# Kernel optimization log

Hardware: AMD Instinct MI355X
Metric: run time of the kernel (lower is better)

## Reference

```python
import jax, jax.numpy as jnp
import numpy as np

B, S, D = 1, 2048, 2048
H = 32          # num_heads == num_kv_heads (n_rep = 1)
QB = 8          # rosa_num_query_key_bits
VB = 8          # rosa_num_value_bits
TAU = 1.0


def setup_inputs() -> dict:
    key = jax.random.key(0)
    ks = jax.random.split(key, 8)
    s = 0.02
    return {
        "hidden_states": jax.random.normal(ks[0], (B, S, D), dtype=jnp.float32),
        "Wq": jax.random.normal(ks[1], (D, H * QB), dtype=jnp.float32) * s,
        "Wk": jax.random.normal(ks[2], (D, H * QB), dtype=jnp.float32) * s,
        "Wv": jax.random.normal(ks[3], (D, H * VB), dtype=jnp.float32) * s,
        "Wo": jax.random.normal(ks[4], (H * VB, D), dtype=jnp.float32) * s,
        "Wg": jax.random.normal(ks[5], (D, D), dtype=jnp.float32) * s,
        "v_emb0": jnp.full((H * VB,), -1e-05, dtype=jnp.float32),
        "v_emb1": jnp.full((H * VB,), +1e-05, dtype=jnp.float32),
    }


def _rosa_attention(hs, Wq, Wk, Wv, Wo, Wg, v_emb0, v_emb1):
    b, s, _ = hs.shape
    # low-bit projections -> [B, H, S, bits]
    q = (hs @ Wq).reshape(b, s, H, QB).transpose(0, 2, 1, 3)
    k = (hs @ Wk).reshape(b, s, H, QB).transpose(0, 2, 1, 3)
    v = (hs @ Wv).reshape(b, s, H, VB).transpose(0, 2, 1, 3)
    # soft-binarized bit probabilities (training-mode relaxation, temperature tau)
    pq = jax.nn.sigmoid(q / TAU)
    pk = jax.nn.sigmoid(k / TAU)
    pv = jax.nn.sigmoid(v / TAU)
    # expected number of matching bits:
    # sum_d pq*pk + (1-pq)*(1-pk) = 2*<pq,pk> - sum(pq) - sum(pk) + QB
    dot = jnp.einsum('bhqd,bhkd->bhqk', pq, pk)
    scores = 2.0 * dot - pq.sum(-1)[..., :, None] - pk.sum(-1)[..., None, :] + QB
    # causal mask
    causal = jnp.tril(jnp.ones((s, s), dtype=bool))
    scores = jnp.where(causal, scores / TAU, jnp.finfo(scores.dtype).min)
    attn = jax.nn.softmax(scores, axis=-1)
    out = jnp.einsum('bhqk,bhkd->bhqd', attn, pv)           # [B,H,S,VB], in (0,1)
    out = out.transpose(0, 2, 1, 3).reshape(b, s, H * VB)
    # binary value-embedding interpolation
    out = v_emb1 * out + v_emb0 * (1.0 - out)
    out = out @ Wo
    gate = jax.nn.sigmoid(hs @ Wg)
    return out * gate


def reference(hidden_states, Wq, Wk, Wv, Wo, Wg, v_emb0, v_emb1):
    return _rosa_attention(hidden_states, Wq, Wk, Wv, Wo, Wg, v_emb0, v_emb1)
```

## Files before the change

### kernel.cpp

```cpp
#include <hip/hip_runtime.h>

#define S 2048
#define DIM 2048
#define H 32
#define NB 2816
#define SA 25.0f
#define SW 1150.0f

using u16 = unsigned short;
using u8 = unsigned char;
using short8 = __attribute__((ext_vector_type(8))) short;
using f32x4 = __attribute__((ext_vector_type(4))) float;
using i32x4 = __attribute__((ext_vector_type(4))) int;

__device__ __forceinline__ u16 f2bf(float x) {
  union { float f; unsigned u; } v; v.f = x;
  unsigned r = v.u + 0x7fffu + ((v.u >> 16) & 1u);
  return (u16)(r >> 16);
}
__device__ __forceinline__ float bf2f(u16 x) {
  union { unsigned u; float f; } v; v.u = ((unsigned)x) << 16; return v.f;
}
__device__ __forceinline__ int clampi(int x) { return x < -127 ? -127 : (x > 127 ? 127 : x); }
__device__ __forceinline__ unsigned q4i8(float a, float b, float c, float d, float s) {
  int x0 = clampi((int)rintf(a * s)), x1 = clampi((int)rintf(b * s));
  int x2 = clampi((int)rintf(c * s)), x3 = clampi((int)rintf(d * s));
  return (x0 & 255) | ((x1 & 255) << 8) | ((x2 & 255) << 16) | ((unsigned)(x3 & 255) << 24);
}

#define GLOAD_LDS16(g, l)                                                      \
  __builtin_amdgcn_global_load_lds(                                            \
      (const __attribute__((address_space(1))) unsigned*)(g),                  \
      (__attribute__((address_space(3))) unsigned*)(l), 16, 0, 0)

__global__ __launch_bounds__(256)
void trans_all_k(const float* __restrict__ Wq, const float* __restrict__ Wk,
                 const float* __restrict__ Wv, const float* __restrict__ Wg,
                 const float* __restrict__ Wo, const float* __restrict__ hs,
                 u16* __restrict__ Wt, u8* __restrict__ Wg8, u16* __restrict__ Wot,
                 u16* __restrict__ Abf, u8* __restrict__ A8) {
  int b = blockIdx.x;
  const int t = threadIdx.x;
  if (b >= 1536) {
    int i = ((b - 1536) * 256 + t) * 8;
    float4 a = *(const float4*)(hs + i);
    float4 c = *(const float4*)(hs + i + 4);
    uint4 r;
    r.x = f2bf(a.x) | ((unsigned)f2bf(a.y) << 16);
    r.y = f2bf(a.z) | ((unsigned)f2bf(a.w) << 16);
    r.z = f2bf(c.x) | ((unsigned)f2bf(c.y) << 16);
    r.w = f2bf(c.z) | ((unsigned)f2bf(c.w) << 16);
    int row = i >> 11, k = i & 2047;
    int dst = (row << 11) + (k & ~63) + ((((k >> 3) & 7) ^ (row & 7)) << 3);
    *(uint4*)(Abf + dst) = r;
    uint2 q;
    q.x = q4i8(a.x, a.y, a.z, a.w, SA);
    q.y = q4i8(c.x, c.y, c.z, c.w, SA);
    int dst8 = (row << 11) + (k & ~63) + ((((k >> 4) & 3) ^ (row & 3)) << 4) + (k & 8);
    *(uint2*)(A8 + dst8) = q;
    return;
  }
  const float* in; int K, N;
  int mode;
  u16* out = nullptr;
  if (b < 384) {
    K = 2048; N = 256; mode = 0;
    in = (b < 128) ? Wq : (b < 256) ? Wk : Wv;
    out = Wt + (size_t)(b >> 7) * 256 * 2048;
    b &= 127;
  } else if (b < 1408) {
    in = Wg; mode = 1; K = 2048; N = 2048; b -= 384;
  } else {
    in = Wo; out = Wot; mode = 2; K = 256; N = 2048; b -= 1408;
  }
  const int nbN = N >> 6;
  const int kb = (b / nbN) << 6, nb = (b % nbN) << 6;
  __shared__ float tile[64][65];
  const int n4 = (t & 15) * 4;
#pragma unroll
  for (int p = 0; p < 4; p++) {
    int k = p * 16 + (t >> 4);
    float4 v = *(const float4*)(in + (size_t)(kb + k) * N + nb + n4);
    tile[k][n4] = v.x; tile[k][n4 + 1] = v.y; tile[k][n4 + 2] = v.z; tile[k][n4 + 3] = v.w;
  }
  __syncthreads();
  const int k8 = (t & 7) * 8;
#pragma unroll
  for (int p = 0; p < 2; p++) {
    int n = p * 32 + (t >> 3);
    if (mode == 1) {
      int nr = nb + n;
      uint2 w;
      w.x = q4i8(tile[k8 + 0][n], tile[k8 + 1][n], tile[k8 + 2][n], tile[k8 + 3][n], SW);
      w.y = q4i8(tile[k8 + 4][n], tile[k8 + 5][n], tile[k8 + 6][n], tile[k8 + 7][n], SW);
      int col = kb + ((((k8 >> 4) ^ (nr & 3))) << 4) + (k8 & 8);
      *(uint2*)(Wg8 + (size_t)nr * 2048 + col) = w;
    } else {
      uint4 w;
      w.x = f2bf(tile[k8 + 0][n]) | ((unsigned)f2bf(tile[k8 + 1][n]) << 16);
      w.y = f2bf(tile[k8 + 2][n]) | ((unsigned)f2bf(tile[k8 + 3][n]) << 16);
      w.z = f2bf(tile[k8 + 4][n]) | ((unsigned)f2bf(tile[k8 + 5][n]) << 16);
      w.w = f2bf(tile[k8 + 6][n]) | ((unsigned)f2bf(tile[k8 + 7][n]) << 16);
      if (mode == 2) {
        *(uint4*)(out + (size_t)(nb + n) * K + kb + k8) = w;
      } else {
        int nr = nb + n;
        int col = kb + ((((k8 >> 3) ^ (nr & 7))) << 3);
        *(uint4*)(out + (size_t)nr * 2048 + col) = w;
      }
    }
  }
}

__global__ __launch_bounds__(256)
void gemm1_mix_k(const u16* __restrict__ Abf, const u16* __restrict__ Wt,
                 const u8* __restrict__ A8, const u8* __restrict__ Wg8,
                 u16* __restrict__ Pb) {
  __shared__ __align__(16) char smem[65536];
  const int t = threadIdx.x;
  const int f = blockIdx.x;
  int bn, bm;
  if (f >= 160 && f < 256) {
    int g = f - 160;
    bn = g % 6;  bm = (g / 6) * 128;
  } else {
    int g = (f < 160) ? f : f - 96;
    bn = 6 + (g & 15);  bm = (g >> 4) * 128;
  }
  const int wave = t >> 6, lane = t & 63;
  const int wm = (wave >> 1) * 64, wn = (wave & 1) * 64;
  const int l16 = lane & 15, quad = lane >> 4;
  const int K = 2048;
  const int srow = t >> 3;
  if (bn < 6) {
    typedef u16 (*Tile)[128][64];
    Tile As = (Tile)smem;
    Tile Bs = (Tile)(smem + 32768);
    const int scol = (t & 7) * 8;
    const u16* Ap = Abf + (size_t)(bm + srow) * K + scol;
    const u16* Bp = Wt + (size_t)(bn * 128 + srow) * K + scol;
#define STAGE1(buf, koff)                                                      \
  do {                                                                         \
    GLOAD_LDS16(Ap + (koff), &As[buf][srow][scol]);                            \
    GLOAD_LDS16(Ap + 32 * (size_t)K + (koff), &As[buf][srow + 32][scol]);      \
    GLOAD_LDS16(Ap + 64 * (size_t)K + (koff), &As[buf][srow + 64][scol]);      \
    GLOAD_LDS16(Ap + 96 * (size_t)K + (koff), &As[buf][srow + 96][scol]);      \
    GLOAD_LDS16(Bp + (koff), &Bs[buf][srow][scol]);                            \
    GLOAD_LDS16(Bp + 32 * (size_t)K + (koff), &Bs[buf][srow + 32][scol]);      \
    GLOAD_LDS16(Bp + 64 * (size_t)K + (koff), &Bs[buf][srow + 64][scol]);      \
    GLOAD_LDS16(Bp + 96 * (size_t)K + (koff), &Bs[buf][srow + 96][scol]);      \
  } while (0)
    f32x4 acc[4][4];
#pragma unroll
    for (int i = 0; i < 4; i++)
#pragma unroll
      for (int j = 0; j < 4; j++) acc[i][j] = (f32x4){0.f, 0.f, 0.f, 0.f};
    STAGE1(0, 0);
    for (int kk = 0; kk < K; kk += 64) {
      const int cur = (kk >> 6) & 1, nxt = cur ^ 1;
      __syncthreads();
      if (kk + 64 < K) STAGE1(nxt, kk + 64);
      short8 af[4][2], bf[4][2];
#pragma unroll
      for (int mt = 0; mt < 4; mt++) {
        int row = wm + mt * 16 + l16;
        int rs = (row & 7) << 3;
        af[mt][0] = *(const short8*)&As[cur][row][(quad << 3) ^ rs];
        af[mt][1] = *(const short8*)&As[cur][row][((quad + 4) << 3) ^ rs];
      }
#pragma unroll
      for (int nt = 0; nt < 4; nt++) {
        int row = wn + nt * 16 + l16;
        int rs = (row & 7) << 3;
        bf[nt][0] = *(const short8*)&Bs[cur][row][(quad << 3) ^ rs];
        bf[nt][1] = *(const short8*)&Bs[cur][row][((quad + 4) << 3) ^ rs];
      }
#pragma unroll
      for (int mt = 0; mt < 4; mt++)
#pragma unroll
        for (int nt = 0; nt < 4; nt++) {
          acc[mt][nt] = __builtin_amdgcn_mfma_f32_16x16x32_bf16(af[mt][0], bf[nt][0], acc[mt][nt], 0, 0, 0);
          acc[mt][nt] = __builtin_amdgcn_mfma_f32_16x16x32_bf16(af[mt][1], bf[nt][1], acc[mt][nt], 0, 0, 0);
        }
    }
#pragma unroll
    for (int mt = 0; mt < 4; mt++)
#pragma unroll
      for (int nt = 0; nt < 4; nt++)
#pragma unroll
        for (int r = 0; r < 4; r++) {
          int m = bm + wm + mt * 16 + quad * 4 + r;
          int n = bn * 128 + wn + nt * 16 + l16;
          float v = acc[mt][nt][r];
          Pb[(size_t)m * NB + n] = f2bf(1.f / (1.f + __expf(-v)));
        }
#undef STAGE1
  } else {
    typedef u8 (*TileG)[128][128];
    TileG As = (TileG)smem;
    TileG Bs = (TileG)(smem + 32768);
    const int scol = (t & 7) * 16;
    const u8* Ap = A8 + (size_t)(bm + srow) * K + scol;
    const u8* Bp = Wg8 + (size_t)((bn - 6) * 128 + srow) * K + scol;
#define STAGEG(buf, koff)                                                      \
  do {                                                                         \
    GLOAD_LDS16(Ap + (koff), &As[buf][srow][scol]);                            \
    GLOAD_LDS16(Ap + 32 * (size_t)K + (koff), &As[buf][srow + 32][scol]);      \
    GLOAD_LDS16(Ap + 64 * (size_t)K + (koff), &As[buf][srow + 64][scol]);      \
    GLOAD_LDS16(Ap + 96 * (size_t)K + (koff), &As[buf][srow + 96][scol]);      \
    GLOAD_LDS16(Bp + (koff), &Bs[buf][srow][scol]);                            \
    GLOAD_LDS16(Bp + 32 * (size_t)K + (koff), &Bs[buf][srow + 32][scol]);      \
    GLOAD_LDS16(Bp + 64 * (size_t)K + (koff), &Bs[buf][srow + 64][scol]);      \
    GLOAD_LDS16(Bp + 96 * (size_t)K + (koff), &Bs[buf][srow + 96][scol]);      \
  } while (0)
    i32x4 acc[4][4];
#pragma unroll
    for (int i = 0; i < 4; i++)
#pragma unroll
      for (int j = 0; j < 4; j++) acc[i][j] = (i32x4){0, 0, 0, 0};
    STAGEG(0, 0);
    for (int kk = 0; kk < K; kk += 128) {
      const int cur = (kk >> 7) & 1, nxt = cur ^ 1;
      __syncthreads();
      if (kk + 128 < K) STAGEG(nxt, kk + 128);
      i32x4 af[4][2], bf[4][2];
#pragma unroll
      for (int mt = 0; mt < 4; mt++) {
        int row = wm + mt * 16 + l16;
        int sl = (quad ^ (row & 3)) << 4;
        af[mt][0] = *(const i32x4*)&As[cur][row][sl];
        af[mt][1] = *(const i32x4*)&As[cur][row][64 + sl];
      }
#pragma unroll
      for (int nt = 0; nt < 4; nt++) {
        int row = wn + nt * 16 + l16;
        int sl = (quad ^ (row & 3)) << 4;
        bf[nt][0] = *(const i32x4*)&Bs[cur][row][sl];
        bf[nt][1] = *(const i32x4*)&Bs[cur][row][64 + sl];
      }
#pragma unroll
      for (int mt = 0; mt < 4; mt++)
#pragma unroll
        for (int nt = 0; nt < 4; nt++) {
          acc[mt][nt] = __builtin_amdgcn_mfma_i32_16x16x64_i8(af[mt][0], bf[nt][0], acc[mt][nt], 0, 0, 0);
          acc[mt][nt] = __builtin_amdgcn_mfma_i32_16x16x64_i8(af[mt][1], bf[nt][1], acc[mt][nt], 0, 0, 0);
        }
    }
    const float inv = 1.f / (SA * SW);
#pragma unroll
    for (int mt = 0; mt < 4; mt++)
#pragma unroll
      for (int nt = 0; nt < 4; nt++)
#pragma unroll
        for (int r = 0; r < 4; r++) {
          int m = bm + wm + mt * 16 + quad * 4 + r;
          int n = bn * 128 + wn + nt * 16 + l16;
          float v = (float)acc[mt][nt][r] * inv;
          Pb[(size_t)m * NB + n] = f2bf(1.f / (1.f + __expf(-v)));
        }
#undef STAGEG
  }
}

__global__ __launch_bounds__(256)
void gemm64_k(const u16* __restrict__ A, const u16* __restrict__ Bt,
              float* __restrict__ C, const u16* __restrict__ gate,
              int K, int ldc) {
  __shared__ u16 As[2][64][32];
  __shared__ u16 Bs[2][64][32];
  const int t = threadIdx.x;
  const int bm = blockIdx.y * 64, bn = blockIdx.x * 64;
  const int wave = t >> 6, lane = t & 63;
  const int wm = (wave >> 1) * 32, wn = (wave & 1) * 32;
  const int l16 = lane & 15, quad = lane >> 4;
  const int srow = t >> 2, scol = (t & 3) * 8;
  const u16* Ap = A + (size_t)(bm + srow) * K + scol;
  const u16* Bp = Bt + (size_t)(bn + srow) * K + scol;
  f32x4 acc[2][2];
#pragma unroll
  for (int i = 0; i < 2; i++)
#pragma unroll
    for (int j = 0; j < 2; j++) acc[i][j] = (f32x4){0.f, 0.f, 0.f, 0.f};
  GLOAD_LDS16(Ap, &As[0][srow][scol]);
  GLOAD_LDS16(Bp, &Bs[0][srow][scol]);
  for (int kk = 0; kk < K; kk += 32) {
    const int cur = (kk >> 5) & 1, nxt = cur ^ 1;
    __syncthreads();
    if (kk + 32 < K) {
      GLOAD_LDS16(Ap + kk + 32, &As[nxt][srow][scol]);
      GLOAD_LDS16(Bp + kk + 32, &Bs[nxt][srow][scol]);
    }
    short8 af[2], bf[2];
#pragma unroll
    for (int mt = 0; mt < 2; mt++) af[mt] = *(const short8*)&As[cur][wm + mt * 16 + l16][quad * 8];
#pragma unroll
    for (int nt = 0; nt < 2; nt++) bf[nt] = *(const short8*)&Bs[cur][wn + nt * 16 + l16][quad * 8];
#pragma unroll
    for (int mt = 0; mt < 2; mt++)
#pragma unroll
      for (int nt = 0; nt < 2; nt++)
        acc[mt][nt] = __builtin_amdgcn_mfma_f32_16x16x32_bf16(af[mt], bf[nt], acc[mt][nt], 0, 0, 0);
  }
#pragma unroll
  for (int mt = 0; mt < 2; mt++)
#pragma unroll
    for (int nt = 0; nt < 2; nt++)
#pragma unroll
      for (int r = 0; r < 4; r++) {
        int m = bm + wm + mt * 16 + quad * 4 + r;
        int n = bn + wn + nt * 16 + l16;
        float v = acc[mt][nt][r] * bf2f(gate[(size_t)m * NB + n]);
        C[(size_t)m * ldc + n] = v;
      }
}

__global__ __launch_bounds__(256)
void attn_mfma_k(const u16* __restrict__ P, float* __restrict__ Part) {
  __shared__ u16 Plds[128 * 128];
  __shared__ u16 Vt[16 * 264];
  __shared__ u16 Klds[256 * 8];
  __shared__ u16 Qlds[128 * 8];
  __shared__ float sk2[256];
  const int h = blockIdx.y;
  int tau = blockIdx.x, m = 0;
  while (tau >= (m >> 1) + 1) { tau -= (m >> 1) + 1; m++; }
  const int kc = tau;
  const bool needMask = (kc == (m >> 1));
  const int q0 = m * 128, kb = kc * 256;
  const int t = threadIdx.x, wave = t >> 6, lane = t & 63;
  const int l16 = lane & 15, quad = lane >> 4;
  if (t < 128) {
    *(uint4*)&Qlds[t * 8] = *(const uint4*)(P + (size_t)(q0 + t) * NB + h * 8);
  }
  {
    const u16* rk = P + (size_t)(kb + t) * NB + 256 + h * 8;
    uint4 wk = *(const uint4*)rk;
    uint4 wv = *(const uint4*)(rk + 256);
    const u16* kv = (const u16*)&wk;
    float sum = 0.f;
#pragma unroll
    for (int d = 0; d < 8; d++) sum += bf2f(kv[d]);
    sk2[t] = sum * 1.44269504f;
    *(uint4*)&Klds[t * 8] = wk;
    const u16* vv = (const u16*)&wv;
#pragma unroll
    for (int d = 0; d < 8; d++) Vt[d * 264 + t] = vv[d];
    Vt[8 * 264 + t] = 0x3F80;
#pragma unroll
    for (int d = 9; d < 16; d++) Vt[d * 264 + t] = 0;
  }
  __syncthreads();
  short8 bq[2];
#pragma unroll
  for (int i = 0; i < 2; i++) {
    short8 z = {0, 0, 0, 0, 0, 0, 0, 0};
    if (quad == 0) z = *(const short8*)&Qlds[((wave * 2 + i) * 16 + l16) * 8];
    bq[i] = z;
  }
  f32x4 O[2];
  O[0] = (f32x4){0.f, 0.f, 0.f, 0.f};
  O[1] = (f32x4){0.f, 0.f, 0.f, 0.f};
  const int nsl = needMask ? (m & 1) + 1 : 2;
  const int swz = (l16 >> 1) & 7;
  for (int sl = 0; sl < nsl; sl++) {
    const int ks = sl * 128;
    const bool dm = needMask && (sl == (m & 1));
    for (int kt = 0; kt < 8; kt++) {
      short8 ak = {0, 0, 0, 0, 0, 0, 0, 0};
      if (quad == 0) ak = *(const short8*)&Klds[(ks + kt * 16 + l16) * 8];
      float4 s2 = *(const float4*)&sk2[ks + kt * 16 + quad * 4];
#pragma unroll
      for (int i = 0; i < 2; i++) {
        f32x4 c = __builtin_amdgcn_mfma_f32_16x16x32_bf16(
            ak, bq[i], (f32x4){0.f, 0.f, 0.f, 0.f}, 0, 0, 0);
        float e0 = exp2f(c[0] * 2.88539008f - s2.x);
        float e1 = exp2f(c[1] * 2.88539008f - s2.y);
        float e2 = exp2f(c[2] * 2.88539008f - s2.z);
        float e3 = exp2f(c[3] * 2.88539008f - s2.w);
        if (dm) {
          int q = q0 + (wave * 2 + i) * 16 + l16;
          int key = kb + ks + kt * 16 + quad * 4;
          e0 = (key + 0 <= q) ? e0 : 0.f;
          e1 = (key + 1 <= q) ? e1 : 0.f;
          e2 = (key + 2 <= q) ? e2 : 0.f;
          e3 = (key + 3 <= q) ? e3 : 0.f;
        }
        uint2 pk2;
        pk2.x = f2bf(e0) | ((unsigned)f2bf(e1) << 16);
        pk2.y = f2bf(e2) | ((unsigned)f2bf(e3) << 16);
        int row = (wave * 2 + i) * 16 + l16;
        int cb = 2 * kt + (quad >> 1);
        int pb = cb ^ swz;
        *(uint2*)&Plds[row * 128 + pb * 8 + (quad & 1) * 4] = pk2;
      }
    }
#pragma unroll
    for (int kc4 = 0; kc4 < 4; kc4++) {
      short8 bv = *(const short8*)&Vt[l16 * 264 + ks + kc4 * 32 + quad * 8];
#pragma unroll
      for (int i = 0; i < 2; i++) {
        int row = (wave * 2 + i) * 16 + l16;
        int pb = (kc4 * 4 + quad) ^ swz;
        short8 ap = *(const short8*)&Plds[row * 128 + pb * 8];
        O[i] = __builtin_amdgcn_mfma_f32_16x16x32_bf16(ap, bv, O[i], 0, 0, 0);
      }
    }
  }
  if (l16 < 9) {
#pragma unroll
    for (int i = 0; i < 2; i++) {
      int qb = q0 + (wave * 2 + i) * 16 + quad * 4;
#pragma unroll
      for (int r = 0; r < 4; r++)
        Part[(((size_t)h * S + qb + r) * 8 + kc) * 12 + l16] = O[i][r];
    }
  }
}

__global__ __launch_bounds__(256)
void attn_merge_k(const float* __restrict__ Part, const float* __restrict__ e0,
                  const float* __restrict__ e1, u16* __restrict__ O2) {
  const int q = blockIdx.x;
  const int t = threadIdx.x;
  const int d = t & 7;
  const int nch = (q >> 8) + 1;
  size_t base = ((size_t)(t >> 3) * S + q) * 8 * 12;
  float ov = 0.f, lv = 0.f;
  for (int kc = 0; kc < nch; kc++) {
    ov += Part[base + (size_t)kc * 12 + d];
    lv += Part[base + (size_t)kc * 12 + 8];
  }
  float outv = ov / lv;
  float r = e0[t] + (e1[t] - e0[t]) * outv;
  O2[(size_t)q * 256 + t] = f2bf(r);
}

extern "C" void kernel_launch(void* const* d_in, const int* in_sizes, int n_in,
                              void* d_out, int out_size, void* d_ws, size_t ws_size,
                              hipStream_t stream) {
  const float* hs = (const float*)d_in[0];
  const float* Wq = (const float*)d_in[1];
  const float* Wk = (const float*)d_in[2];
  const float* Wv = (const float*)d_in[3];
  const float* Wo = (const float*)d_in[4];
  const float* Wg = (const float*)d_in[5];
  const float* e0 = (const float*)d_in[6];
  const float* e1 = (const float*)d_in[7];
  float* out = (float*)d_out;
  char* ws = (char*)d_ws;
  u16*   Abf  = (u16*)(ws + 0);
  u8*    A8   = (u8*)(ws + 8388608);
  u16*   Wt   = (u16*)(ws + 12582912);
  u8*    Wg8  = (u8*)(ws + 15728640);
  u16*   Wot  = (u16*)(ws + 19922944);
  u16*   O2   = (u16*)(ws + 20971520);
  u16*   Pb   = (u16*)(ws + 22020096);
  float* Part = (float*)(ws + 33554432);

  trans_all_k<<<dim3(3584), 256, 0, stream>>>(Wq, Wk, Wv, Wg, Wo, hs, Wt, Wg8, Wot, Abf, A8);
  gemm1_mix_k<<<dim3(352), 256, 0, stream>>>(Abf, Wt, A8, Wg8, Pb);
  attn_mfma_k<<<dim3(72, H), 256, 0, stream>>>(Pb, Part);
  attn_merge_k<<<dim3(S), 256, 0, stream>>>(Part, e0, e1, O2);
  gemm64_k<<<dim3(DIM / 64, S / 64), 256, 0, stream>>>(O2, Wot, out, Pb + 768, 256, DIM);
}
```

Measured before the change: 168.5 us.

## Fuse attention split-K partials and merge into single kernel with in-block K loop

Replaces the split-K attention kernel plus separate merge kernel with one kernel where each block loops over all key chunks for its 128-query tile and head, accumulating in registers. The final normalization and value-embedding interpolation are done in-kernel using a lane shuffle to fetch the row-sum column. Blocks are ordered so the heaviest query tiles launch first. This removes the partial-sum buffer writes/reads and one kernel launch, but cuts the grid from 2304 to 512 blocks with uneven per-block work, which lowers parallelism and may leave the GPU underfilled.

```diff
diff --git a/kernel.cpp b/kernel.cpp
--- a/kernel.cpp
+++ b/kernel.cpp
@@ -315,40 +315,22 @@
 }
 
 __global__ __launch_bounds__(256)
-void attn_mfma_k(const u16* __restrict__ P, float* __restrict__ Part) {
+void attn_fused_k(const u16* __restrict__ P, const float* __restrict__ e0,
+                  const float* __restrict__ e1, u16* __restrict__ O2) {
   __shared__ u16 Plds[128 * 128];
   __shared__ u16 Vt[16 * 264];
   __shared__ u16 Klds[256 * 8];
   __shared__ u16 Qlds[128 * 8];
   __shared__ float sk2[256];
-  const int h = blockIdx.y;
-  int tau = blockIdx.x, m = 0;
-  while (tau >= (m >> 1) + 1) { tau -= (m >> 1) + 1; m++; }
-  const int kc = tau;
-  const bool needMask = (kc == (m >> 1));
-  const int q0 = m * 128, kb = kc * 256;
+  const int f = blockIdx.x;
+  int h, m;
+  if (f < 256) { h = f >> 3; m = 8 + (f & 7); }
+  else         { int g = f - 256; h = g >> 3; m = 7 - (g & 7); }
+  const int q0 = m * 128;
   const int t = threadIdx.x, wave = t >> 6, lane = t & 63;
   const int l16 = lane & 15, quad = lane >> 4;
-  if (t < 128) {
+  if (t < 128)
     *(uint4*)&Qlds[t * 8] = *(const uint4*)(P + (size_t)(q0 + t) * NB + h * 8);
-  }
-  {
-    const u16* rk = P + (size_t)(kb + t) * NB + 256 + h * 8;
-    uint4 wk = *(const uint4*)rk;
-    uint4 wv = *(const uint4*)(rk + 256);
-    const u16* kv = (const u16*)&wk;
-    float sum = 0.f;
-#pragma unroll
-    for (int d = 0; d < 8; d++) sum += bf2f(kv[d]);
-    sk2[t] = sum * 1.44269504f;
-    *(uint4*)&Klds[t * 8] = wk;
-    const u16* vv = (const u16*)&wv;
-#pragma unroll
-    for (int d = 0; d < 8; d++) Vt[d * 264 + t] = vv[d];
-    Vt[8 * 264 + t] = 0x3F80;
-#pragma unroll
-    for (int d = 9; d < 16; d++) Vt[d * 264 + t] = 0;
-  }
   __syncthreads();
   short8 bq[2];
 #pragma unroll
@@ -360,79 +342,90 @@
   f32x4 O[2];
   O[0] = (f32x4){0.f, 0.f, 0.f, 0.f};
   O[1] = (f32x4){0.f, 0.f, 0.f, 0.f};
-  const int nsl = needMask ? (m & 1) + 1 : 2;
   const int swz = (l16 >> 1) & 7;
-  for (int sl = 0; sl < nsl; sl++) {
-    const int ks = sl * 128;
-    const bool dm = needMask && (sl == (m & 1));
-    for (int kt = 0; kt < 8; kt++) {
-      short8 ak = {0, 0, 0, 0, 0, 0, 0, 0};
-      if (quad == 0) ak = *(const short8*)&Klds[(ks + kt * 16 + l16) * 8];
-      float4 s2 = *(const float4*)&sk2[ks + kt * 16 + quad * 4];
-#pragma unroll
-      for (int i = 0; i < 2; i++) {
-        f32x4 c = __builtin_amdgcn_mfma_f32_16x16x32_bf16(
-            ak, bq[i], (f32x4){0.f, 0.f, 0.f, 0.f}, 0, 0, 0);
-        float e0 = exp2f(c[0] * 2.88539008f - s2.x);
-        float e1 = exp2f(c[1] * 2.88539008f - s2.y);
-        float e2 = exp2f(c[2] * 2.88539008f - s2.z);
-        float e3 = exp2f(c[3] * 2.88539008f - s2.w);
-        if (dm) {
-          int q = q0 + (wave * 2 + i) * 16 + l16;
-          int key = kb + ks + kt * 16 + quad * 4;
-          e0 = (key + 0 <= q) ? e0 : 0.f;
-          e1 = (key + 1 <= q) ? e1 : 0.f;
-          e2 = (key + 2 <= q) ? e2 : 0.f;
-          e3 = (key + 3 <= q) ? e3 : 0.f;
-        }
-        uint2 pk2;
-        pk2.x = f2bf(e0) | ((unsigned)f2bf(e1) << 16);
-        pk2.y = f2bf(e2) | ((unsigned)f2bf(e3) << 16);
-        int row = (wave * 2 + i) * 16 + l16;
-        int cb = 2 * kt + (quad >> 1);
-        int pb = cb ^ swz;
-        *(uint2*)&Plds[row * 128 + pb * 8 + (quad & 1) * 4] = pk2;
-      }
-    }
-#pragma unroll
-    for (int kc4 = 0; kc4 < 4; kc4++) {
-      short8 bv = *(const short8*)&Vt[l16 * 264 + ks + kc4 * 32 + quad * 8];
-#pragma unroll
-      for (int i = 0; i < 2; i++) {
-        int row = (wave * 2 + i) * 16 + l16;
-        int pb = (kc4 * 4 + quad) ^ swz;
-        short8 ap = *(const short8*)&Plds[row * 128 + pb * 8];
-        O[i] = __builtin_amdgcn_mfma_f32_16x16x32_bf16(ap, bv, O[i], 0, 0, 0);
-      }
-    }
-  }
-  if (l16 < 9) {
-#pragma unroll
-    for (int i = 0; i < 2; i++) {
-      int qb = q0 + (wave * 2 + i) * 16 + quad * 4;
-#pragma unroll
-      for (int r = 0; r < 4; r++)
-        Part[(((size_t)h * S + qb + r) * 8 + kc) * 12 + l16] = O[i][r];
-    }
-  }
-}
-
-__global__ __launch_bounds__(256)
-void attn_merge_k(const float* __restrict__ Part, const float* __restrict__ e0,
-                  const float* __restrict__ e1, u16* __restrict__ O2) {
-  const int q = blockIdx.x;
-  const int t = threadIdx.x;
-  const int d = t & 7;
-  const int nch = (q >> 8) + 1;
-  size_t base = ((size_t)(t >> 3) * S + q) * 8 * 12;
-  float ov = 0.f, lv = 0.f;
-  for (int kc = 0; kc < nch; kc++) {
-    ov += Part[base + (size_t)kc * 12 + d];
-    lv += Part[base + (size_t)kc * 12 + 8];
-  }
-  float outv = ov / lv;
-  float r = e0[t] + (e1[t] - e0[t]) * outv;
-  O2[(size_t)q * 256 + t] = f2bf(r);
+  const int nkc = (m >> 1) + 1;
+  for (int kc = 0; kc < nkc; kc++) {
+    const int kb = kc * 256;
+    const bool needMask = (kc == (m >> 1));
+    if (kc) __syncthreads();
+    {
+      const u16* rk = P + (size_t)(kb + t) * NB + 256 + h * 8;
+      uint4 wk = *(const uint4*)rk;
+      uint4 wv = *(const uint4*)(rk + 256);
+      const u16* kv = (const u16*)&wk;
+      float sum = 0.f;
+#pragma unroll
+      for (int d = 0; d < 8; d++) sum += bf2f(kv[d]);
+      sk2[t] = sum * 1.44269504f;
+      *(uint4*)&Klds[t * 8] = wk;
+      const u16* vv = (const u16*)&wv;
+#pragma unroll
+      for (int d = 0; d < 8; d++) Vt[d * 264 + t] = vv[d];
+      Vt[8 * 264 + t] = 0x3F80;
+#pragma unroll
+      for (int d = 9; d < 16; d++) Vt[d * 264 + t] = 0;
+    }
+    __syncthreads();
+    const int nsl = needMask ? (m & 1) + 1 : 2;
+    for (int sl = 0; sl < nsl; sl++) {
+      const int ks = sl * 128;
+      const bool dm = needMask && (sl == (m & 1));
+      for (int kt = 0; kt < 8; kt++) {
+        short8 ak = {0, 0, 0, 0, 0, 0, 0, 0};
+        if (quad == 0) ak = *(const short8*)&Klds[(ks + kt * 16 + l16) * 8];
+        float4 s2 = *(const float4*)&sk2[ks + kt * 16 + quad * 4];
+#pragma unroll
+        for (int i = 0; i < 2; i++) {
+          f32x4 c = __builtin_amdgcn_mfma_f32_16x16x32_bf16(
+              ak, bq[i], (f32x4){0.f, 0.f, 0.f, 0.f}, 0, 0, 0);
+          float e0v = exp2f(c[0] * 2.88539008f - s2.x);
+          float e1v = exp2f(c[1] * 2.88539008f - s2.y);
+          float e2v = exp2f(c[2] * 2.88539008f - s2.z);
+          float e3v = exp2f(c[3] * 2.88539008f - s2.w);
+          if (dm) {
+            int q = q0 + (wave * 2 + i) * 16 + l16;
+            int key = kb + ks + kt * 16 + quad * 4;
+            e0v = (key + 0 <= q) ? e0v : 0.f;
+            e1v = (key + 1 <= q) ? e1v : 0.f;
+            e2v = (key + 2 <= q) ? e2v : 0.f;
+            e3v = (key + 3 <= q) ? e3v : 0.f;
+          }
+          uint2 pk2;
+          pk2.x = f2bf(e0v) | ((unsigned)f2bf(e1v) << 16);
+          pk2.y = f2bf(e2v) | ((unsigned)f2bf(e3v) << 16);
+          int row = (wave * 2 + i) * 16 + l16;
+          int cb = 2 * kt + (quad >> 1);
+          int pb = cb ^ swz;
+          *(uint2*)&Plds[row * 128 + pb * 8 + (quad & 1) * 4] = pk2;
+        }
+      }
+#pragma unroll
+      for (int kc4 = 0; kc4 < 4; kc4++) {
+        short8 bv = *(const short8*)&Vt[l16 * 264 + ks + kc4 * 32 + quad * 8];
+#pragma unroll
+        for (int i = 0; i < 2; i++) {
+          int row = (wave * 2 + i) * 16 + l16;
+          int pb = (kc4 * 4 + quad) ^ swz;
+          short8 ap = *(const short8*)&Plds[row * 128 + pb * 8];
+          O[i] = __builtin_amdgcn_mfma_f32_16x16x32_bf16(ap, bv, O[i], 0, 0, 0);
+        }
+      }
+    }
+  }
+  float ev0 = 0.f, ev1 = 0.f;
+  if (l16 < 8) { ev0 = e0[h * 8 + l16]; ev1 = e1[h * 8 + l16]; }
+#pragma unroll
+  for (int i = 0; i < 2; i++) {
+#pragma unroll
+    for (int r = 0; r < 4; r++) {
+      float lv = __shfl(O[i][r], quad * 16 + 8, 64);
+      if (l16 < 8) {
+        int q = q0 + (wave * 2 + i) * 16 + quad * 4 + r;
+        float outv = O[i][r] / lv;
+        O2[(size_t)q * 256 + h * 8 + l16] = f2bf(ev0 + (ev1 - ev0) * outv);
+      }
+    }
+  }
 }
 
 extern "C" void kernel_launch(void* const* d_in, const int* in_sizes, int n_in,
@@ -455,11 +448,9 @@
   u16*   Wot  = (u16*)(ws + 19922944);
   u16*   O2   = (u16*)(ws + 20971520);
   u16*   Pb   = (u16*)(ws + 22020096);
-  float* Part = (float*)(ws + 33554432);
 
   trans_all_k<<<dim3(3584), 256, 0, stream>>>(Wq, Wk, Wv, Wg, Wo, hs, Wt, Wg8, Wot, Abf, A8);
   gemm1_mix_k<<<dim3(352), 256, 0, stream>>>(Abf, Wt, A8, Wg8, Pb);
-  attn_mfma_k<<<dim3(72, H), 256, 0, stream>>>(Pb, Part);
-  attn_merge_k<<<dim3(S), 256, 0, stream>>>(Part, e0, e1, O2);
+  attn_fused_k<<<dim3(512), 256, 0, stream>>>(Pb, e0, e1, O2);
   gemm64_k<<<dim3(DIM / 64, S / 64), 256, 0, stream>>>(O2, Wot, out, Pb + 768, 256, DIM);
 }
```

After: 182.0 us. +8.0%, slower.
